# Kernel tuning notes

Measured on AMD Instinct MI355X. Metric: run time of the kernel, lower is better.

The kernel has to match this reference:

```python
import jax, jax.numpy as jnp
import numpy as np

_INT8_MM_MIN_M = 32


def setup_inputs() -> dict:
    key = jax.random.key(0)
    k1, k2, k3, k4 = jax.random.split(key, 4)
    M, K, N = 8192, 4096, 11008
    x = jax.random.normal(k1, (M, K), dtype=jnp.float32)
    # int8 weight in K-major [K, N] layout, symmetric range
    qweight = jax.random.randint(k2, (K, N), -127, 128, dtype=jnp.int32).astype(jnp.int8)
    weight_scale = jax.random.uniform(k3, (N,), dtype=jnp.float32, minval=1e-3, maxval=2e-2)
    input_scale = jax.random.uniform(k4, (1,), dtype=jnp.float32, minval=1e-2, maxval=5e-2)
    return {"x": x, "qweight": qweight, "weight_scale": weight_scale, "input_scale": input_scale}


def reference(x, qweight, weight_scale, input_scale):
    """w8a8_static path of Int8LinearBase (M > 32 branch, no bias).

    x: [M, K] float32; qweight: [K, N] int8; weight_scale: [N]; input_scale: [1].
    """
    M = x.shape[0]
    # static activation quantization: div -> clamp -> round -> int8
    x_int8 = jnp.round(jnp.clip(x / input_scale, -128.0, 127.0)).astype(jnp.int8)
    # pad M up to a multiple of _INT8_MM_MIN_M (cuBLAS alignment workaround)
    pad_m = (_INT8_MM_MIN_M - M % _INT8_MM_MIN_M) % _INT8_MM_MIN_M
    if M <= 16:
        pad_m = _INT8_MM_MIN_M - M
    if pad_m > 0:
        x_int8 = jnp.pad(x_int8, ((0, pad_m), (0, 0)))
    out_i32 = jnp.matmul(x_int8, qweight, preferred_element_type=jnp.int32)[:M]  # [M, N]
    # fused dequant: per-tensor input scale * per-channel weight scale
    out = out_i32.astype(jnp.float32) * input_scale * weight_scale[None, :]
    return out
```

## Files before the change

kernel.cpp:

```cpp
#include <hip/hip_runtime.h>
#include <hip/hip_bf16.h>

typedef int v4i __attribute__((ext_vector_type(4)));

#define GLOBAL_AS(p) ((const __attribute__((address_space(1))) void*)(p))
#define LDS_AS(p)    ((__attribute__((address_space(3))) void*)(p))

#define BM 128
#define BN 128
#define BK 64

__global__ __launch_bounds__(256) void quant_kernel(
    const float* __restrict__ x, signed char* __restrict__ xq,
    const float* __restrict__ iscale, int n4)
{
    int idx = blockIdx.x * 256 + threadIdx.x;
    if (idx >= n4) return;
    float s = iscale[0];
    float4 v = ((const float4*)x)[idx];
    int b0 = (int)rintf(fminf(fmaxf(v.x / s, -128.f), 127.f));
    int b1 = (int)rintf(fminf(fmaxf(v.y / s, -128.f), 127.f));
    int b2 = (int)rintf(fminf(fmaxf(v.z / s, -128.f), 127.f));
    int b3 = (int)rintf(fminf(fmaxf(v.w / s, -128.f), 127.f));
    unsigned packed = (unsigned)(b0 & 255) | ((unsigned)(b1 & 255) << 8) |
                      ((unsigned)(b2 & 255) << 16) | ((unsigned)(b3 & 255) << 24);
    ((unsigned*)xq)[idx] = packed;
}

__global__ __launch_bounds__(256) void transpose_kernel(
    const int* __restrict__ in, signed char* __restrict__ out,
    int K, int N)
{
    __shared__ unsigned char t[64][68];
    const int n0 = blockIdx.x * 64;
    const int k0 = blockIdx.y * 64;
    const int tid = threadIdx.x;

#pragma unroll
    for (int i = 0; i < 4; i++) {
        int d = tid + i * 256;
        int r = d >> 4, c = d & 15;
        int4 v = *(const int4*)(in + (size_t)(k0 + r) * N + n0 + c * 4);
        unsigned o = (unsigned)(v.x & 255) | ((unsigned)(v.y & 255) << 8) |
                     ((unsigned)(v.z & 255) << 16) | ((unsigned)(v.w & 255) << 24);
        *(unsigned*)&t[r][c * 4] = o;
    }
    __syncthreads();
#pragma unroll
    for (int i = 0; i < 4; i++) {
        int d = tid + i * 256;
        int n = d >> 4, b = d & 15;
        unsigned o = (unsigned)t[4 * b + 0][n]
                   | ((unsigned)t[4 * b + 1][n] << 8)
                   | ((unsigned)t[4 * b + 2][n] << 16)
                   | ((unsigned)t[4 * b + 3][n] << 24);
        *(unsigned*)(out + (size_t)(n0 + n) * K + k0 + b * 4) = o;
    }
}

__global__ __launch_bounds__(256) void gemm_i8_kernel(
    const signed char* __restrict__ A,
    const signed char* __restrict__ Bt,
    float* __restrict__ out,
    const float* __restrict__ wscale,
    const float* __restrict__ iscale,
    int M, int N, int K)
{
    __shared__ __align__(16) signed char lA[BM * BK];
    __shared__ __align__(16) signed char lB[BN * BK];

    const int tid  = threadIdx.x;
    const int wave = tid >> 6;
    const int lane = tid & 63;
    const int bm = blockIdx.x;
    const int bn = blockIdx.y;

    const int c0 = wave * 2;
    const signed char* gA0 = A  + (size_t)(bm * BM + c0 * 16 + (lane >> 2)) * K + (lane & 3) * 16;
    const signed char* gA1 = gA0 + (size_t)16 * K;
    const signed char* gB0 = Bt + (size_t)(bn * BN + c0 * 16 + (lane >> 2)) * K + (lane & 3) * 16;
    const signed char* gB1 = gB0 + (size_t)16 * K;
    void* ldsA0 = (void*)&lA[c0 * 1024];
    void* ldsA1 = (void*)&lA[c0 * 1024 + 1024];
    void* ldsB0 = (void*)&lB[c0 * 1024];
    void* ldsB1 = (void*)&lB[c0 * 1024 + 1024];

    const int wm = (wave >> 1) * 64;
    const int wn = (wave & 1) * 64;
    const int row16 = lane & 15;
    const int quad  = lane >> 4;
    const int aoff = (wm + row16) * 64 + quad * 16;
    const int boff = (wn + row16) * 64 + quad * 16;

    v4i acc[4][4] = {};

    for (int k0 = 0; k0 < K; k0 += BK) {
        __syncthreads();
        __builtin_amdgcn_global_load_lds(GLOBAL_AS(gA0), LDS_AS(ldsA0), 16, 0, 0);
        __builtin_amdgcn_global_load_lds(GLOBAL_AS(gA1), LDS_AS(ldsA1), 16, 0, 0);
        __builtin_amdgcn_global_load_lds(GLOBAL_AS(gB0), LDS_AS(ldsB0), 16, 0, 0);
        __builtin_amdgcn_global_load_lds(GLOBAL_AS(gB1), LDS_AS(ldsB1), 16, 0, 0);
        gA0 += BK; gA1 += BK; gB0 += BK; gB1 += BK;
        __syncthreads();

        v4i af[4], bf[4];
#pragma unroll
        for (int mi = 0; mi < 4; mi++)
            af[mi] = *(const v4i*)&lA[aoff + mi * 1024];
#pragma unroll
        for (int ni = 0; ni < 4; ni++)
            bf[ni] = *(const v4i*)&lB[boff + ni * 1024];
#pragma unroll
        for (int mi = 0; mi < 4; mi++)
#pragma unroll
            for (int ni = 0; ni < 4; ni++)
                acc[mi][ni] = __builtin_amdgcn_mfma_i32_16x16x64_i8(
                    af[mi], bf[ni], acc[mi][ni], 0, 0, 0);
    }

    const float isc = iscale[0];
#pragma unroll
    for (int ni = 0; ni < 4; ni++) {
        const int ncol = bn * BN + wn + ni * 16 + row16;
        const float sc = isc * wscale[ncol];
        float* obase = out + (size_t)(bm * BM + wm + quad * 4) * N + ncol;
#pragma unroll
        for (int mi = 0; mi < 4; mi++) {
#pragma unroll
            for (int r = 0; r < 4; r++) {
                obase[(size_t)(mi * 16 + r) * N] = (float)acc[mi][ni][r] * sc;
            }
        }
    }
}

extern "C" void kernel_launch(void* const* d_in, const int* in_sizes, int n_in,
                              void* d_out, int out_size, void* d_ws, size_t ws_size,
                              hipStream_t stream) {
    const float* x      = (const float*)d_in[0];
    const int*   qw     = (const int*)d_in[1];
    const float* wscale = (const float*)d_in[2];
    const float* iscale = (const float*)d_in[3];
    float*       out    = (float*)d_out;

    const int N = in_sizes[2];
    const int K = in_sizes[1] / N;
    const int M = in_sizes[0] / K;

    signed char* xq  = (signed char*)d_ws;
    signed char* qwT = (signed char*)d_ws + (size_t)M * K;

    {
        int n4 = (M * K) / 4;
        quant_kernel<<<(n4 + 255) / 256, 256, 0, stream>>>(x, xq, iscale, n4);
    }
    {
        dim3 grid(N / 64, K / 64);
        transpose_kernel<<<grid, 256, 0, stream>>>(qw, qwT, K, N);
    }
    {
        dim3 grid(M / BM, N / BN);
        gemm_i8_kernel<<<grid, 256, 0, stream>>>(xq, qwT, out, wscale, iscale, M, N, K);
    }
}
```

Before: 1.043 ms.

## Rewrite int8 GEMM with 256x256 tiles, 4-stage LDS pipeline and XCD swizzle

Replaces the 128x128 single-buffered GEMM with a 256x256 tile, 512-thread block and a 4-stage global_load_lds ring. Loads for future K tiles are issued while MFMAs run, with raised wave priority during MFMA phases. Blocks are remapped across XCDs so that neighbouring tiles share L2. LDS reads use an XOR swizzle to reduce bank conflicts. The cost is much higher LDS use per block (128KB) and more accumulator registers, which limits occupancy.

```diff
diff --git a/kernel.cpp b/kernel.cpp
--- a/kernel.cpp
+++ b/kernel.cpp
@@ -1,14 +1,9 @@
 #include <hip/hip_runtime.h>
-#include <hip/hip_bf16.h>
 
 typedef int v4i __attribute__((ext_vector_type(4)));
 
 #define GLOBAL_AS(p) ((const __attribute__((address_space(1))) void*)(p))
 #define LDS_AS(p)    ((__attribute__((address_space(3))) void*)(p))
-
-#define BM 128
-#define BN 128
-#define BK 64
 
 __global__ __launch_bounds__(256) void quant_kernel(
     const float* __restrict__ x, signed char* __restrict__ xq,
@@ -58,7 +53,56 @@
     }
 }
 
-__global__ __launch_bounds__(256) void gemm_i8_kernel(
+#define BM 256
+#define BN 256
+#define BK 64
+
+#define STAGE_A(ss, kk) do { \
+    __builtin_amdgcn_global_load_lds(GLOBAL_AS(pA0 + (kk)), LDS_AS(&lA[ss][stg0]), 16, 0, 0); \
+    __builtin_amdgcn_global_load_lds(GLOBAL_AS(pA1 + (kk)), LDS_AS(&lA[ss][stg1]), 16, 0, 0); \
+} while (0)
+
+#define STAGE_B(ss, kk) do { \
+    __builtin_amdgcn_global_load_lds(GLOBAL_AS(pB0 + (kk)), LDS_AS(&lB[ss][stg0]), 16, 0, 0); \
+    __builtin_amdgcn_global_load_lds(GLOBAL_AS(pB1 + (kk)), LDS_AS(&lB[ss][stg1]), 16, 0, 0); \
+} while (0)
+
+#define TILE(j) do { \
+    const int ss = (j); const int sp = ((j) + 3) & 3; \
+    int kpre = (t0 + (j) + 3) << 6; \
+    if (kpre >= K) kpre -= K;    \
+    const signed char* pa = &lA[ss][aoffL]; \
+    const signed char* pb = &lB[ss][boffL]; \
+    v4i aF0[4], aF1[4], bF[4]; \
+     \
+    _Pragma("unroll") for (int i = 0; i < 4; ++i) aF0[i] = *(const v4i*)(pa + i * 1024); \
+    _Pragma("unroll") for (int i = 0; i < 4; ++i) bF[i]  = *(const v4i*)(pb + i * 1024); \
+    STAGE_A(sp, kpre); \
+    __builtin_amdgcn_s_barrier(); \
+    asm volatile("s_waitcnt lgkmcnt(0)" ::: "memory"); \
+    __builtin_amdgcn_sched_barrier(0); \
+    __builtin_amdgcn_s_setprio(1); \
+    _Pragma("unroll") for (int mi = 0; mi < 4; ++mi) \
+        _Pragma("unroll") for (int ni = 0; ni < 4; ++ni) \
+            acc[mi][ni] = __builtin_amdgcn_mfma_i32_16x16x64_i8(aF0[mi], bF[ni], acc[mi][ni], 0, 0, 0); \
+    __builtin_amdgcn_s_setprio(0); \
+    __builtin_amdgcn_s_barrier(); \
+     \
+    _Pragma("unroll") for (int i = 0; i < 4; ++i) aF1[i] = *(const v4i*)(pa + (4 + i) * 1024); \
+    STAGE_B(sp, kpre); \
+    __builtin_amdgcn_s_barrier(); \
+    asm volatile("s_waitcnt lgkmcnt(0)" ::: "memory"); \
+    __builtin_amdgcn_sched_barrier(0); \
+    __builtin_amdgcn_s_setprio(1); \
+    _Pragma("unroll") for (int mi = 0; mi < 4; ++mi) \
+        _Pragma("unroll") for (int ni = 0; ni < 4; ++ni) \
+            acc[4 + mi][ni] = __builtin_amdgcn_mfma_i32_16x16x64_i8(aF1[mi], bF[ni], acc[4 + mi][ni], 0, 0, 0); \
+    __builtin_amdgcn_s_setprio(0); \
+    asm volatile("s_waitcnt vmcnt(8)" ::: "memory");   \
+    __builtin_amdgcn_s_barrier(); \
+} while (0)
+
+__global__ __launch_bounds__(512, 2) void gemm_i8_kernel(
     const signed char* __restrict__ A,
     const signed char* __restrict__ Bt,
     float* __restrict__ out,
@@ -66,69 +110,67 @@
     const float* __restrict__ iscale,
     int M, int N, int K)
 {
-    __shared__ __align__(16) signed char lA[BM * BK];
-    __shared__ __align__(16) signed char lB[BN * BK];
+    __shared__ __align__(16) signed char lA[4][BM * BK];
+    __shared__ __align__(16) signed char lB[4][BN * BK];
 
     const int tid  = threadIdx.x;
     const int wave = tid >> 6;
     const int lane = tid & 63;
-    const int bm = blockIdx.x;
-    const int bn = blockIdx.y;
-
-    const int c0 = wave * 2;
-    const signed char* gA0 = A  + (size_t)(bm * BM + c0 * 16 + (lane >> 2)) * K + (lane & 3) * 16;
-    const signed char* gA1 = gA0 + (size_t)16 * K;
-    const signed char* gB0 = Bt + (size_t)(bn * BN + c0 * 16 + (lane >> 2)) * K + (lane & 3) * 16;
-    const signed char* gB1 = gB0 + (size_t)16 * K;
-    void* ldsA0 = (void*)&lA[c0 * 1024];
-    void* ldsA1 = (void*)&lA[c0 * 1024 + 1024];
-    void* ldsB0 = (void*)&lB[c0 * 1024];
-    void* ldsB1 = (void*)&lB[c0 * 1024 + 1024];
-
-    const int wm = (wave >> 1) * 64;
-    const int wn = (wave & 1) * 64;
-    const int row16 = lane & 15;
-    const int quad  = lane >> 4;
-    const int aoff = (wm + row16) * 64 + quad * 16;
-    const int boff = (wn + row16) * 64 + quad * 16;
-
-    v4i acc[4][4] = {};
-
-    for (int k0 = 0; k0 < K; k0 += BK) {
-        __syncthreads();
-        __builtin_amdgcn_global_load_lds(GLOBAL_AS(gA0), LDS_AS(ldsA0), 16, 0, 0);
-        __builtin_amdgcn_global_load_lds(GLOBAL_AS(gA1), LDS_AS(ldsA1), 16, 0, 0);
-        __builtin_amdgcn_global_load_lds(GLOBAL_AS(gB0), LDS_AS(ldsB0), 16, 0, 0);
-        __builtin_amdgcn_global_load_lds(GLOBAL_AS(gB1), LDS_AS(ldsB1), 16, 0, 0);
-        gA0 += BK; gA1 += BK; gB0 += BK; gB1 += BK;
-        __syncthreads();
-
-        v4i af[4], bf[4];
-#pragma unroll
-        for (int mi = 0; mi < 4; mi++)
-            af[mi] = *(const v4i*)&lA[aoff + mi * 1024];
-#pragma unroll
-        for (int ni = 0; ni < 4; ni++)
-            bf[ni] = *(const v4i*)&lB[boff + ni * 1024];
-#pragma unroll
-        for (int mi = 0; mi < 4; mi++)
-#pragma unroll
-            for (int ni = 0; ni < 4; ni++)
-                acc[mi][ni] = __builtin_amdgcn_mfma_i32_16x16x64_i8(
-                    af[mi], bf[ni], acc[mi][ni], 0, 0, 0);
+
+    const int nwg = gridDim.x;
+    const int q = nwg >> 3, r = nwg & 7;
+    const int xcd = blockIdx.x & 7, o = blockIdx.x >> 3;
+    const int swz = (xcd < r ? xcd * (q + 1) : r * (q + 1) + (xcd - r) * q) + o;
+    const int nbm = M >> 8;
+    const int bm = swz % nbm;
+    const int bn = swz / nbm;
+
+    const int srow = tid >> 2;
+    const int scol = ((tid & 3) ^ ((tid >> 3) & 3)) << 4;
+    const signed char* pA0 = A  + (size_t)((bm << 8) + srow) * K + scol;
+    const signed char* pA1 = pA0 + (size_t)128 * K;
+    const signed char* pB0 = Bt + (size_t)((bn << 8) + srow) * K + scol;
+    const signed char* pB1 = pB0 + (size_t)128 * K;
+    const int stg0 = wave << 10;
+    const int stg1 = 8192 + (wave << 10);
+
+    const int r15  = lane & 15;
+    const int quad = lane >> 4;
+    const int wm = (wave >> 2) << 7;
+    const int wn = (wave & 3) << 6;
+    const int swzs = (r15 >> 1) & 3;
+    const int aoffL = (wm + r15) * 64 + ((quad ^ swzs) << 4);
+    const int boffL = (wn + r15) * 64 + ((quad ^ swzs) << 4);
+
+    v4i acc[8][4] = {};
+
+    STAGE_A(0, 0);   STAGE_B(0, 0);
+    STAGE_A(1, 64);  STAGE_B(1, 64);
+    STAGE_A(2, 128); STAGE_B(2, 128);
+    asm volatile("s_waitcnt vmcnt(8)" ::: "memory");
+    __builtin_amdgcn_s_barrier();
+
+    const int NT = K >> 6;
+#pragma unroll 1
+    for (int t0 = 0; t0 < NT; t0 += 4) {
+        TILE(0);
+        TILE(1);
+        TILE(2);
+        TILE(3);
     }
 
     const float isc = iscale[0];
-#pragma unroll
-    for (int ni = 0; ni < 4; ni++) {
-        const int ncol = bn * BN + wn + ni * 16 + row16;
+    const int orow = (bm << 8) + wm + (quad << 2);
+#pragma unroll
+    for (int ni = 0; ni < 4; ++ni) {
+        const int ncol = (bn << 8) + wn + ni * 16 + r15;
         const float sc = isc * wscale[ncol];
-        float* obase = out + (size_t)(bm * BM + wm + quad * 4) * N + ncol;
-#pragma unroll
-        for (int mi = 0; mi < 4; mi++) {
-#pragma unroll
-            for (int r = 0; r < 4; r++) {
-                obase[(size_t)(mi * 16 + r) * N] = (float)acc[mi][ni][r] * sc;
+        float* obase = out + (size_t)orow * N + ncol;
+#pragma unroll
+        for (int mi = 0; mi < 8; ++mi) {
+#pragma unroll
+            for (int rr = 0; rr < 4; ++rr) {
+                obase[(size_t)(mi * 16 + rr) * N] = (float)acc[mi][ni][rr] * sc;
             }
         }
     }
@@ -159,7 +201,7 @@
         transpose_kernel<<<grid, 256, 0, stream>>>(qw, qwT, K, N);
     }
     {
-        dim3 grid(M / BM, N / BN);
-        gemm_i8_kernel<<<grid, 256, 0, stream>>>(xq, qwT, out, wscale, iscale, M, N, K);
-    }
-}
+        int nwg = (M >> 8) * (N >> 8);
+        gemm_i8_kernel<<<nwg, 512, 0, stream>>>(xq, qwT, out, wscale, iscale, M, N, K);
+    }
+}
```

Measured after the change: 1.028 ms. No clear change (-1.5%).
